# Kernel tuning notes

Measured on AMD Instinct MI355X. Metric: run time of the kernel, lower is better.

The kernel has to match this reference:

```python
import jax, jax.numpy as jnp
import numpy as np

B, S, D = 4, 1568, 1024
H = 16
HD = D // H  # 64


def setup_inputs() -> dict:
    key = jax.random.key(0)
    ks = jax.random.split(key, 9)
    scale = 0.02
    return {
        "hidden_states": jax.random.normal(ks[0], (B, S, D), dtype=jnp.float32),
        "Wq": jax.random.normal(ks[1], (D, D), dtype=jnp.float32) * scale,
        "bq": jnp.zeros((D,), dtype=jnp.float32),
        "Wk": jax.random.normal(ks[2], (D, D), dtype=jnp.float32) * scale,
        "bk": jnp.zeros((D,), dtype=jnp.float32),
        "Wv": jax.random.normal(ks[3], (D, D), dtype=jnp.float32) * scale,
        "bv": jnp.zeros((D,), dtype=jnp.float32),
        "Wp": jax.random.normal(ks[4], (D, D), dtype=jnp.float32) * scale,
        "bp": jnp.zeros((D,), dtype=jnp.float32),
    }


def reference(hidden_states, Wq, bq, Wk, bk, Wv, bv, Wp, bp):
    x = hidden_states  # [B, S, D]
    # Linear projections (torch Linear: x @ W.T + b)
    q = x @ Wq.T + bq
    k = x @ Wk.T + bk
    v = x @ Wv.T + bv
    # split heads: [B, H, S, HD]
    def heads(t):
        return t.reshape(B, S, H, HD).transpose(0, 2, 1, 3)
    q, k, v = heads(q), heads(k), heads(v)
    scale = 1.0 / jnp.sqrt(jnp.asarray(HD, dtype=q.dtype))
    scores = jnp.einsum('bhqd,bhkd->bhqk', q, k) * scale  # [B,H,S,S]
    probs = jax.nn.softmax(scores, axis=-1)
    ctx = jnp.einsum('bhqk,bhkd->bhqd', probs, v)  # [B,H,S,HD]
    ctx = ctx.transpose(0, 2, 1, 3).reshape(B, S, D)
    out = ctx @ Wp.T + bp
    return out
```

## Files before the change

### kernel.cpp

```cpp
#include <hip/hip_runtime.h>
#include <stdint.h>

#define SEQ 1568
#define SEQV 1600
#define DIM 1024
#define NB 4
#define NH 16
#define HD 64

typedef unsigned short u16;
typedef __bf16 bf16x8 __attribute__((ext_vector_type(8)));
typedef __bf16 bf16x4 __attribute__((ext_vector_type(4)));
typedef float f32x4 __attribute__((ext_vector_type(4)));

#define QSCALE 0.18033688011112042f

#define PSTR 72

__device__ __forceinline__ void load_lds16(const u16* g, u16* s) {
  __builtin_amdgcn_global_load_lds((__attribute__((address_space(1))) void*)g,
                                   (__attribute__((address_space(3))) void*)s,
                                   16, 0, 0);
}

#define WAIT_VM(N) asm volatile("s_waitcnt vmcnt(" #N ")" ::: "memory")
#define LGKM0()    asm volatile("s_waitcnt lgkmcnt(0)" ::: "memory")
#define BAR()      do { __builtin_amdgcn_s_barrier(); \
                        __builtin_amdgcn_sched_barrier(0); } while (0)

__global__ __launch_bounds__(256) void cvt_all(
    const float* __restrict__ x,  const float* __restrict__ wq,
    const float* __restrict__ wk, const float* __restrict__ wv,
    const float* __restrict__ wp,
    u16* __restrict__ xb, u16* __restrict__ wqb, u16* __restrict__ wkb,
    u16* __restrict__ wvb, u16* __restrict__ wpb) {
  int i = blockIdx.x * 256 + threadIdx.x;
  const float* src; u16* dst; int off;
  if (i < 1605632)      { src = x;  dst = xb;  off = i; }
  else if (i < 1867776) { src = wq; dst = wqb; off = i - 1605632; }
  else if (i < 2129920) { src = wk; dst = wkb; off = i - 1867776; }
  else if (i < 2392064) { src = wv; dst = wvb; off = i - 2129920; }
  else                  { src = wp; dst = wpb; off = i - 2392064; }
  float4 v = ((const float4*)src)[off];
  union { unsigned long long u; __bf16 h[4]; } o;
  o.h[0] = (__bf16)v.x; o.h[1] = (__bf16)v.y;
  o.h[2] = (__bf16)v.z; o.h[3] = (__bf16)v.w;
  ((unsigned long long*)dst)[off] = o.u;
}

__global__ __launch_bounds__(256) void gemm_qkv(
    const u16* __restrict__ xb,
    const u16* __restrict__ wq, const u16* __restrict__ wk, const u16* __restrict__ wv,
    const float* __restrict__ bq, const float* __restrict__ bk, const float* __restrict__ bv,
    u16* __restrict__ qo, u16* __restrict__ ko, u16* __restrict__ vto) {
  const int bid = blockIdx.x + (blockIdx.y << 3) + blockIdx.z * 416;
  const int logical = (bid & 7) * 156 + (bid >> 3);
  const int byz = logical >> 3;
  const int by  = byz % 52;
  const int z   = byz / 52;
  const int bi  = by / 13;
  const int st  = by % 13;
  const int bn  = (logical & 7) * 128;

  const u16* W = (z == 0) ? wq : (z == 1) ? wk : wv;
  const float* bias = (z == 0) ? bq : (z == 1) ? bk : bv;

  __shared__ __align__(16) u16 sA[3][128 * 32];
  __shared__ __align__(16) u16 sB[3][128 * 32];

  const int tid = threadIdx.x;
  const int wave = tid >> 6;
  const int lane = tid & 63;
  const int l15 = lane & 15;
  const int quad = lane >> 4;
  const int wm = (wave >> 1) * 64;
  const int wn = (wave & 1) * 64;

  const int sr  = lane >> 2;
  const int scs = (((lane & 3) ^ ((lane >> 3) & 3)) << 3);
  const int r0 = wave * 32;

  int ra1 = st * 128 + r0 + sr;       if (ra1 >= SEQ) ra1 = SEQ - 1;
  int ra2 = st * 128 + r0 + 16 + sr;  if (ra2 >= SEQ) ra2 = SEQ - 1;
  const u16* gA1 = xb + (size_t)(bi * SEQ + ra1) * DIM + scs;
  const u16* gA2 = xb + (size_t)(bi * SEQ + ra2) * DIM + scs;
  const u16* gB1 = W + (size_t)(bn + r0 + sr) * DIM + scs;
  const u16* gB2 = gB1 + 16 * DIM;

  f32x4 acc[4][4] = {};
  const int rsw = (l15 >> 1) & 3;

  auto stage = [&](int kk, u16* sAc, u16* sBc) {
    load_lds16(gA1 + kk, sAc + r0 * 32);
    load_lds16(gA2 + kk, sAc + (r0 + 16) * 32);
    load_lds16(gB1 + kk, sBc + r0 * 32);
    load_lds16(gB2 + kk, sBc + (r0 + 16) * 32);
  };

  auto mstep = [&](const u16* sAc, const u16* sBc) {
    bf16x8 a[4], b[4];
#pragma unroll
    for (int mt = 0; mt < 4; mt++)
      a[mt] = *(const bf16x8*)&sAc[(wm + mt * 16 + l15) * 32 + ((quad ^ rsw) << 3)];
#pragma unroll
    for (int nt = 0; nt < 4; nt++)
      b[nt] = *(const bf16x8*)&sBc[(wn + nt * 16 + l15) * 32 + ((quad ^ rsw) << 3)];
#pragma unroll
    for (int mt = 0; mt < 4; mt++)
#pragma unroll
      for (int nt = 0; nt < 4; nt++)
        acc[mt][nt] = __builtin_amdgcn_mfma_f32_16x16x32_bf16(a[mt], b[nt], acc[mt][nt], 0, 0, 0);
  };

  stage(0,  &sA[0][0], &sB[0][0]);
  stage(32, &sA[1][0], &sB[1][0]);
  stage(64, &sA[2][0], &sB[2][0]);

#pragma unroll 1
  for (int t = 0; t < 30; t += 3) {
    WAIT_VM(8); BAR();
    mstep(&sA[0][0], &sB[0][0]);
    LGKM0(); BAR();
    stage((t + 3) * 32, &sA[0][0], &sB[0][0]);

    WAIT_VM(8); BAR();
    mstep(&sA[1][0], &sB[1][0]);
    LGKM0(); BAR();
    stage((t + 4) * 32, &sA[1][0], &sB[1][0]);

    WAIT_VM(8); BAR();
    mstep(&sA[2][0], &sB[2][0]);
    LGKM0(); BAR();
    if (t + 5 < 32) stage((t + 5) * 32, &sA[2][0], &sB[2][0]);
  }
  WAIT_VM(4); BAR();
  mstep(&sA[0][0], &sB[0][0]);
  WAIT_VM(0); BAR();
  mstep(&sA[1][0], &sB[1][0]);

#pragma unroll
  for (int nt = 0; nt < 4; nt++) {
    const int n = bn + wn + nt * 16 + l15;
    const float bia = bias[n];
    const int h = n >> 6, d = n & 63;
#pragma unroll
    for (int mt = 0; mt < 4; mt++) {
      const int sbase = st * 128 + wm + mt * 16 + quad * 4;
#pragma unroll
      for (int r = 0; r < 4; r++) {
        const int s = sbase + r;
        if (s < SEQ) {
          float val = acc[mt][nt][r] + bia;
          if (z == 0) val *= QSCALE;
          const __bf16 o = (__bf16)val;
          if (z == 0)
            *(__bf16*)&qo[(((size_t)(bi * NH + h)) * SEQ + s) * HD + d] = o;
          else if (z == 1)
            *(__bf16*)&ko[(((size_t)(bi * NH + h)) * SEQ + s) * HD + d] = o;
          else
            *(__bf16*)&vto[(((size_t)(bi * NH + h)) * HD + d) * SEQV + s] = o;
        }
      }
    }
  }
}

__global__ __launch_bounds__(256, 3) void attn(
    const u16* __restrict__ q, const u16* __restrict__ k,
    const u16* __restrict__ vt, u16* __restrict__ ctx) {
  const int bid = blockIdx.x;
  const int logical = (bid & 7) * 104 + (bid >> 3);
  const int bh = logical / 13;
  const int qt = logical % 13;
  const int tid = threadIdx.x;
  const int wave = tid >> 6, lane = tid & 63, l15 = lane & 15, quad = lane >> 4;

  __shared__ __align__(16) u16 sK[2][64 * 64];
  __shared__ __align__(16) u16 sV[2][64 * 64];
  __shared__ __align__(16) u16 sP[4][32 * PSTR];

  const u16* qh = q + (size_t)bh * (SEQ * HD);
  const u16* kh = k + (size_t)bh * (SEQ * HD);
  const u16* vh = vt + (size_t)bh * (HD * SEQV);

  bf16x8 aq[2][2];
#pragma unroll
  for (int mt = 0; mt < 2; mt++) {
    int qrow = qt * 128 + wave * 32 + mt * 16 + l15;
    int qr = qrow < SEQ ? qrow : SEQ - 1;
    aq[mt][0] = *(const bf16x8*)&qh[(size_t)qr * HD + quad * 8];
    aq[mt][1] = *(const bf16x8*)&qh[(size_t)qr * HD + 32 + quad * 8];
  }

  f32x4 o[2][4] = {};
  float lsum[2] = {0.0f, 0.0f};

  const int jrow = lane >> 3;
  const int cg = (lane & 7) ^ jrow;
  u16* sPw = sP[wave];
  const int j7 = l15 & 7;
  const int d7 = l15 & 7;

  auto stageKV = [&](int t, int b) {
    const int j0 = t * 64;
    int kr1 = j0 + wave * 16 + jrow;      if (kr1 >= SEQ) kr1 = SEQ - 1;
    int kr2 = j0 + wave * 16 + 8 + jrow;  if (kr2 >= SEQ) kr2 = SEQ - 1;
    load_lds16(&kh[(size_t)kr1 * HD + cg * 8], &sK[b][(wave * 16) * 64]);
    load_lds16(&kh[(size_t)kr2 * HD + cg * 8], &sK[b][(wave * 16 + 8) * 64]);
    load_lds16(&vh[(size_t)(wave * 16 + jrow) * SEQV + j0 + cg * 8], &sV[b][(wave * 16) * 64]);
    load_lds16(&vh[(size_t)(wave * 16 + 8 + jrow) * SEQV + j0 + cg * 8], &sV[b][(wave * 16 + 8) * 64]);
  };

  auto compute_full = [&](int b) {
    const u16* sKc = sK[b];
    const u16* sVc = sV[b];
#pragma unroll
    for (int mt = 0; mt < 2; mt++) {
      f32x4 s[4];
#pragma unroll
      for (int jt = 0; jt < 4; jt++) {
        const int j = jt * 16 + l15;
        bf16x8 b0 = *(const bf16x8*)&sKc[j * 64 + ((quad ^ j7) * 8)];
        bf16x8 b1 = *(const bf16x8*)&sKc[j * 64 + (((4 + quad) ^ j7) * 8)];
        f32x4 acc = {};
        acc = __builtin_amdgcn_mfma_f32_16x16x32_bf16(b0, aq[mt][0], acc, 0, 0, 0);
        acc = __builtin_amdgcn_mfma_f32_16x16x32_bf16(b1, aq[mt][1], acc, 0, 0, 0);
        s[jt] = acc;
      }
#pragma unroll
      for (int jt = 0; jt < 4; jt++) {
        bf16x4 pk;
#pragma unroll
        for (int r = 0; r < 4; r++) {
          float p = __builtin_exp2f(s[jt][r]);
          lsum[mt] += p;
          pk[r] = (__bf16)p;
        }
        *(bf16x4*)&sPw[(mt * 16 + l15) * PSTR + jt * 16 + quad * 4] = pk;
      }
    }

    LGKM0();

#pragma unroll
    for (int kc = 0; kc < 2; kc++) {
      bf16x8 ap0 = *(const bf16x8*)&sPw[l15 * PSTR + kc * 32 + quad * 8];
      bf16x8 ap1 = *(const bf16x8*)&sPw[(16 + l15) * PSTR + kc * 32 + quad * 8];
#pragma unroll
      for (int dt = 0; dt < 4; dt++) {
        bf16x8 bv = *(const bf16x8*)&sVc[(dt * 16 + l15) * 64 + (((kc * 4 + quad) ^ d7) * 8)];
        o[0][dt] = __builtin_amdgcn_mfma_f32_16x16x32_bf16(ap0, bv, o[0][dt], 0, 0, 0);
        o[1][dt] = __builtin_amdgcn_mfma_f32_16x16x32_bf16(ap1, bv, o[1][dt], 0, 0, 0);
      }
    }
  };

  auto compute_tail = [&](int b) {
    const u16* sKc = sK[b];
    const u16* sVc = sV[b];
#pragma unroll
    for (int mt = 0; mt < 2; mt++) {
      f32x4 s[2];
#pragma unroll
      for (int jt = 0; jt < 2; jt++) {
        const int j = jt * 16 + l15;
        bf16x8 b0 = *(const bf16x8*)&sKc[j * 64 + ((quad ^ j7) * 8)];
        bf16x8 b1 = *(const bf16x8*)&sKc[j * 64 + (((4 + quad) ^ j7) * 8)];
        f32x4 acc = {};
        acc = __builtin_amdgcn_mfma_f32_16x16x32_bf16(b0, aq[mt][0], acc, 0, 0, 0);
        acc = __builtin_amdgcn_mfma_f32_16x16x32_bf16(b1, aq[mt][1], acc, 0, 0, 0);
        s[jt] = acc;
      }
#pragma unroll
      for (int jt = 0; jt < 2; jt++) {
        bf16x4 pk;
#pragma unroll
        for (int r = 0; r < 4; r++) {
          float p = __builtin_exp2f(s[jt][r]);
          lsum[mt] += p;
          pk[r] = (__bf16)p;
        }
        *(bf16x4*)&sPw[(mt * 16 + l15) * PSTR + jt * 16 + quad * 4] = pk;
      }
    }

    LGKM0();

    {
      bf16x8 ap0 = *(const bf16x8*)&sPw[l15 * PSTR + quad * 8];
      bf16x8 ap1 = *(const bf16x8*)&sPw[(16 + l15) * PSTR + quad * 8];
#pragma unroll
      for (int dt = 0; dt < 4; dt++) {
        bf16x8 bv = *(const bf16x8*)&sVc[(dt * 16 + l15) * 64 + ((quad ^ d7) * 8)];
        o[0][dt] = __builtin_amdgcn_mfma_f32_16x16x32_bf16(ap0, bv, o[0][dt], 0, 0, 0);
        o[1][dt] = __builtin_amdgcn_mfma_f32_16x16x32_bf16(ap1, bv, o[1][dt], 0, 0, 0);
      }
    }
  };

  stageKV(0, 0);
#pragma unroll 1
  for (int t = 0; t < 25; t++) {
    if (t < 24) {
      stageKV(t + 1, (t + 1) & 1);
      WAIT_VM(4);
    } else {
      WAIT_VM(0);
    }
    BAR();
    if (t < 24) compute_full(t & 1);
    else        compute_tail(t & 1);
    BAR();
  }

  const int bi = bh >> 4, h = bh & 15;
  float Lq[2][4];
#pragma unroll
  for (int mt = 0; mt < 2; mt++) {
    float l = lsum[mt];
    l += __shfl_xor(l, 16);
    l += __shfl_xor(l, 32);
#pragma unroll
    for (int r = 0; r < 4; r++)
      Lq[mt][r] = __shfl(l, quad * 4 + r, 16);
  }
#pragma unroll
  for (int mt = 0; mt < 2; mt++) {
#pragma unroll
    for (int r = 0; r < 4; r++) {
      const int srow = qt * 128 + wave * 32 + mt * 16 + quad * 4 + r;
      if (srow < SEQ) {
        const float inv = 1.0f / Lq[mt][r];
#pragma unroll
        for (int dt = 0; dt < 4; dt++)
          *(__bf16*)&ctx[((size_t)(bi * SEQ + srow)) * DIM + h * HD + dt * 16 + l15] =
              (__bf16)(o[mt][dt][r] * inv);
      }
    }
  }
}

__global__ __launch_bounds__(256) void gemm_out(
    const u16* __restrict__ ctx, const u16* __restrict__ wp,
    const float* __restrict__ bp, float* __restrict__ out) {
  const int bid = blockIdx.x;
  const int logical = (bid & 7) * 49 + (bid >> 3);
  const int bm = (logical >> 3) * 128;
  const int bn = (logical & 7) * 128;

  __shared__ __align__(16) u16 sA[3][128 * 32];
  __shared__ __align__(16) u16 sB[3][128 * 32];

  const int tid = threadIdx.x;
  const int wave = tid >> 6;
  const int lane = tid & 63;
  const int l15 = lane & 15;
  const int quad = lane >> 4;
  const int wm = (wave >> 1) * 64;
  const int wn = (wave & 1) * 64;
  const int sr  = lane >> 2;
  const int scs = (((lane & 3) ^ ((lane >> 3) & 3)) << 3);
  const int r0 = wave * 32;

  const u16* gA1 = ctx + (size_t)(bm + r0 + sr) * DIM + scs;
  const u16* gA2 = gA1 + 16 * DIM;
  const u16* gB1 = wp + (size_t)(bn + r0 + sr) * DIM + scs;
  const u16* gB2 = gB1 + 16 * DIM;

  f32x4 acc[4][4] = {};
  const int rsw = (l15 >> 1) & 3;

  auto stage = [&](int kk, u16* sAc, u16* sBc) {
    load_lds16(gA1 + kk, sAc + r0 * 32);
    load_lds16(gA2 + kk, sAc + (r0 + 16) * 32);
    load_lds16(gB1 + kk, sBc + r0 * 32);
    load_lds16(gB2 + kk, sBc + (r0 + 16) * 32);
  };

  auto mstep = [&](const u16* sAc, const u16* sBc) {
    bf16x8 a[4], b[4];
#pragma unroll
    for (int mt = 0; mt < 4; mt++)
      a[mt] = *(const bf16x8*)&sAc[(wm + mt * 16 + l15) * 32 + ((quad ^ rsw) << 3)];
#pragma unroll
    for (int nt = 0; nt < 4; nt++)
      b[nt] = *(const bf16x8*)&sBc[(wn + nt * 16 + l15) * 32 + ((quad ^ rsw) << 3)];
#pragma unroll
    for (int mt = 0; mt < 4; mt++)
#pragma unroll
      for (int nt = 0; nt < 4; nt++)
        acc[mt][nt] = __builtin_amdgcn_mfma_f32_16x16x32_bf16(a[mt], b[nt], acc[mt][nt], 0, 0, 0);
  };

  stage(0,  &sA[0][0], &sB[0][0]);
  stage(32, &sA[1][0], &sB[1][0]);
  stage(64, &sA[2][0], &sB[2][0]);

#pragma unroll 1
  for (int t = 0; t < 30; t += 3) {
    WAIT_VM(8); BAR();
    mstep(&sA[0][0], &sB[0][0]);
    LGKM0(); BAR();
    stage((t + 3) * 32, &sA[0][0], &sB[0][0]);

    WAIT_VM(8); BAR();
    mstep(&sA[1][0], &sB[1][0]);
    LGKM0(); BAR();
    stage((t + 4) * 32, &sA[1][0], &sB[1][0]);

    WAIT_VM(8); BAR();
    mstep(&sA[2][0], &sB[2][0]);
    LGKM0(); BAR();
    if (t + 5 < 32) stage((t + 5) * 32, &sA[2][0], &sB[2][0]);
  }
  WAIT_VM(4); BAR();
  mstep(&sA[0][0], &sB[0][0]);
  WAIT_VM(0); BAR();
  mstep(&sA[1][0], &sB[1][0]);

#pragma unroll
  for (int nt = 0; nt < 4; nt++) {
    const int n = bn + wn + nt * 16 + l15;
    const float bia = bp[n];
#pragma unroll
    for (int mt = 0; mt < 4; mt++) {
      const int mbase = bm + wm + mt * 16 + quad * 4;
#pragma unroll
      for (int r = 0; r < 4; r++)
        out[(size_t)(mbase + r) * DIM + n] = acc[mt][nt][r] + bia;
    }
  }
}

extern "C" void kernel_launch(void* const* d_in, const int* in_sizes, int n_in,
                              void* d_out, int out_size, void* d_ws, size_t ws_size,
                              hipStream_t stream) {
  const float* x  = (const float*)d_in[0];
  const float* Wq = (const float*)d_in[1];
  const float* bq = (const float*)d_in[2];
  const float* Wk = (const float*)d_in[3];
  const float* bk = (const float*)d_in[4];
  const float* Wv = (const float*)d_in[5];
  const float* bv = (const float*)d_in[6];
  const float* Wp = (const float*)d_in[7];
  const float* bp = (const float*)d_in[8];
  float* out = (float*)d_out;

  char* ws = (char*)d_ws;
  u16* xb   = (u16*)(ws + 0);
  u16* wqb  = (u16*)(ws + 12845056);
  u16* wkb  = (u16*)(ws + 14942208);
  u16* wvb  = (u16*)(ws + 17039360);
  u16* wpb  = (u16*)(ws + 19136512);
  u16* qb   = (u16*)(ws + 21233664);
  u16* kb   = (u16*)(ws + 34078720);
  u16* vtb  = (u16*)(ws + 46923776);
  u16* ctxb = (u16*)(ws + 60030976);

  cvt_all<<<10368, 256, 0, stream>>>(x, Wq, Wk, Wv, Wp, xb, wqb, wkb, wvb, wpb);
  gemm_qkv<<<dim3(8, 52, 3), 256, 0, stream>>>(xb, wqb, wkb, wvb, bq, bk, bv, qb, kb, vtb);
  attn<<<832, 256, 0, stream>>>(qb, kb, vtb, ctxb);
  gemm_out<<<392, 256, 0, stream>>>(ctxb, wpb, bp, out);
}
```

Before: 293.8 us.

## Flatten QKV GEMM rows across batch; single-buffer attention KV with higher occupancy

The QKV projection now tiles over the flattened B*S rows (6272 = 49*128), which removes padded partial tiles per batch and drops the row clamping and bounds checks. Each output row is mapped back to (batch, seq) for the head-split stores. Attention drops double-buffered K/V LDS staging for a single buffer with plain syncthreads, raises launch bounds to 4 blocks per CU, and adds s_setprio around the MFMA sections. The aim is less padding waste and more occupancy to hide latency, at the cost of losing explicit load/compute overlap inside each block.

```diff
diff --git a/kernel.cpp b/kernel.cpp
--- a/kernel.cpp
+++ b/kernel.cpp
@@ -53,14 +53,12 @@
     const u16* __restrict__ wq, const u16* __restrict__ wk, const u16* __restrict__ wv,
     const float* __restrict__ bq, const float* __restrict__ bk, const float* __restrict__ bv,
     u16* __restrict__ qo, u16* __restrict__ ko, u16* __restrict__ vto) {
-  const int bid = blockIdx.x + (blockIdx.y << 3) + blockIdx.z * 416;
-  const int logical = (bid & 7) * 156 + (bid >> 3);
-  const int byz = logical >> 3;
-  const int by  = byz % 52;
-  const int z   = byz / 52;
-  const int bi  = by / 13;
-  const int st  = by % 13;
-  const int bn  = (logical & 7) * 128;
+  const int bid = blockIdx.x;
+  const int logical = (bid & 7) * 147 + (bid >> 3);
+  const int z   = logical / 392;
+  const int rem = logical % 392;
+  const int bm  = (rem >> 3) * 128;
+  const int bn  = (rem & 7) * 128;
 
   const u16* W = (z == 0) ? wq : (z == 1) ? wk : wv;
   const float* bias = (z == 0) ? bq : (z == 1) ? bk : bv;
@@ -80,10 +78,8 @@
   const int scs = (((lane & 3) ^ ((lane >> 3) & 3)) << 3);
   const int r0 = wave * 32;
 
-  int ra1 = st * 128 + r0 + sr;       if (ra1 >= SEQ) ra1 = SEQ - 1;
-  int ra2 = st * 128 + r0 + 16 + sr;  if (ra2 >= SEQ) ra2 = SEQ - 1;
-  const u16* gA1 = xb + (size_t)(bi * SEQ + ra1) * DIM + scs;
-  const u16* gA2 = xb + (size_t)(bi * SEQ + ra2) * DIM + scs;
+  const u16* gA1 = xb + (size_t)(bm + r0 + sr) * DIM + scs;
+  const u16* gA2 = gA1 + 16 * DIM;
   const u16* gB1 = W + (size_t)(bn + r0 + sr) * DIM + scs;
   const u16* gB2 = gB1 + 16 * DIM;
 
@@ -145,27 +141,27 @@
     const int h = n >> 6, d = n & 63;
 #pragma unroll
     for (int mt = 0; mt < 4; mt++) {
-      const int sbase = st * 128 + wm + mt * 16 + quad * 4;
+      const int rbase = bm + wm + mt * 16 + quad * 4;
 #pragma unroll
       for (int r = 0; r < 4; r++) {
-        const int s = sbase + r;
-        if (s < SEQ) {
-          float val = acc[mt][nt][r] + bia;
-          if (z == 0) val *= QSCALE;
-          const __bf16 o = (__bf16)val;
-          if (z == 0)
-            *(__bf16*)&qo[(((size_t)(bi * NH + h)) * SEQ + s) * HD + d] = o;
-          else if (z == 1)
-            *(__bf16*)&ko[(((size_t)(bi * NH + h)) * SEQ + s) * HD + d] = o;
-          else
-            *(__bf16*)&vto[(((size_t)(bi * NH + h)) * HD + d) * SEQV + s] = o;
-        }
-      }
-    }
-  }
-}
-
-__global__ __launch_bounds__(256, 3) void attn(
+        const int row = rbase + r;
+        const int bi = row / SEQ;
+        const int s  = row - bi * SEQ;
+        float val = acc[mt][nt][r] + bia;
+        if (z == 0) val *= QSCALE;
+        const __bf16 o = (__bf16)val;
+        if (z == 0)
+          *(__bf16*)&qo[(((size_t)(bi * NH + h)) * SEQ + s) * HD + d] = o;
+        else if (z == 1)
+          *(__bf16*)&ko[(((size_t)(bi * NH + h)) * SEQ + s) * HD + d] = o;
+        else
+          *(__bf16*)&vto[(((size_t)(bi * NH + h)) * HD + d) * SEQV + s] = o;
+      }
+    }
+  }
+}
+
+__global__ __launch_bounds__(256, 4) void attn(
     const u16* __restrict__ q, const u16* __restrict__ k,
     const u16* __restrict__ vt, u16* __restrict__ ctx) {
   const int bid = blockIdx.x;
@@ -175,8 +171,8 @@
   const int tid = threadIdx.x;
   const int wave = tid >> 6, lane = tid & 63, l15 = lane & 15, quad = lane >> 4;
 
-  __shared__ __align__(16) u16 sK[2][64 * 64];
-  __shared__ __align__(16) u16 sV[2][64 * 64];
+  __shared__ __align__(16) u16 sK[64 * 64];
+  __shared__ __align__(16) u16 sV[64 * 64];
   __shared__ __align__(16) u16 sP[4][32 * PSTR];
 
   const u16* qh = q + (size_t)bh * (SEQ * HD);
@@ -199,34 +195,30 @@
   const int cg = (lane & 7) ^ jrow;
   u16* sPw = sP[wave];
   const int j7 = l15 & 7;
-  const int d7 = l15 & 7;
-
-  auto stageKV = [&](int t, int b) {
-    const int j0 = t * 64;
-    int kr1 = j0 + wave * 16 + jrow;      if (kr1 >= SEQ) kr1 = SEQ - 1;
-    int kr2 = j0 + wave * 16 + 8 + jrow;  if (kr2 >= SEQ) kr2 = SEQ - 1;
-    load_lds16(&kh[(size_t)kr1 * HD + cg * 8], &sK[b][(wave * 16) * 64]);
-    load_lds16(&kh[(size_t)kr2 * HD + cg * 8], &sK[b][(wave * 16 + 8) * 64]);
-    load_lds16(&vh[(size_t)(wave * 16 + jrow) * SEQV + j0 + cg * 8], &sV[b][(wave * 16) * 64]);
-    load_lds16(&vh[(size_t)(wave * 16 + 8 + jrow) * SEQV + j0 + cg * 8], &sV[b][(wave * 16 + 8) * 64]);
-  };
-
-  auto compute_full = [&](int b) {
-    const u16* sKc = sK[b];
-    const u16* sVc = sV[b];
+
+  for (int j0 = 0; j0 < 1536; j0 += 64) {
+    __syncthreads();
+    load_lds16(&kh[(size_t)(j0 + wave * 16 + jrow) * HD + cg * 8], &sK[(wave * 16) * 64]);
+    load_lds16(&kh[(size_t)(j0 + wave * 16 + 8 + jrow) * HD + cg * 8], &sK[(wave * 16 + 8) * 64]);
+    load_lds16(&vh[(size_t)(wave * 16 + jrow) * SEQV + j0 + cg * 8], &sV[(wave * 16) * 64]);
+    load_lds16(&vh[(size_t)(wave * 16 + 8 + jrow) * SEQV + j0 + cg * 8], &sV[(wave * 16 + 8) * 64]);
+    __syncthreads();
+
 #pragma unroll
     for (int mt = 0; mt < 2; mt++) {
       f32x4 s[4];
+      __builtin_amdgcn_s_setprio(1);
 #pragma unroll
       for (int jt = 0; jt < 4; jt++) {
         const int j = jt * 16 + l15;
-        bf16x8 b0 = *(const bf16x8*)&sKc[j * 64 + ((quad ^ j7) * 8)];
-        bf16x8 b1 = *(const bf16x8*)&sKc[j * 64 + (((4 + quad) ^ j7) * 8)];
+        bf16x8 b0 = *(const bf16x8*)&sK[j * 64 + ((quad ^ j7) * 8)];
+        bf16x8 b1 = *(const bf16x8*)&sK[j * 64 + (((4 + quad) ^ j7) * 8)];
         f32x4 acc = {};
         acc = __builtin_amdgcn_mfma_f32_16x16x32_bf16(b0, aq[mt][0], acc, 0, 0, 0);
         acc = __builtin_amdgcn_mfma_f32_16x16x32_bf16(b1, aq[mt][1], acc, 0, 0, 0);
         s[jt] = acc;
       }
+      __builtin_amdgcn_s_setprio(0);
 #pragma unroll
       for (int jt = 0; jt < 4; jt++) {
         bf16x4 pk;
@@ -242,30 +234,41 @@
 
     LGKM0();
 
+    __builtin_amdgcn_s_setprio(1);
 #pragma unroll
     for (int kc = 0; kc < 2; kc++) {
       bf16x8 ap0 = *(const bf16x8*)&sPw[l15 * PSTR + kc * 32 + quad * 8];
       bf16x8 ap1 = *(const bf16x8*)&sPw[(16 + l15) * PSTR + kc * 32 + quad * 8];
 #pragma unroll
       for (int dt = 0; dt < 4; dt++) {
-        bf16x8 bv = *(const bf16x8*)&sVc[(dt * 16 + l15) * 64 + (((kc * 4 + quad) ^ d7) * 8)];
+        const int d7 = l15 & 7;
+        bf16x8 bv = *(const bf16x8*)&sV[(dt * 16 + l15) * 64 + (((kc * 4 + quad) ^ d7) * 8)];
         o[0][dt] = __builtin_amdgcn_mfma_f32_16x16x32_bf16(ap0, bv, o[0][dt], 0, 0, 0);
         o[1][dt] = __builtin_amdgcn_mfma_f32_16x16x32_bf16(ap1, bv, o[1][dt], 0, 0, 0);
       }
     }
-  };
-
-  auto compute_tail = [&](int b) {
-    const u16* sKc = sK[b];
-    const u16* sVc = sV[b];
+    __builtin_amdgcn_s_setprio(0);
+  }
+
+  {
+    const int j0 = 1536;
+    __syncthreads();
+    if (wave < 2) {
+      load_lds16(&kh[(size_t)(j0 + wave * 16 + jrow) * HD + cg * 8], &sK[(wave * 16) * 64]);
+      load_lds16(&kh[(size_t)(j0 + wave * 16 + 8 + jrow) * HD + cg * 8], &sK[(wave * 16 + 8) * 64]);
+    }
+    load_lds16(&vh[(size_t)(wave * 16 + jrow) * SEQV + j0 + cg * 8], &sV[(wave * 16) * 64]);
+    load_lds16(&vh[(size_t)(wave * 16 + 8 + jrow) * SEQV + j0 + cg * 8], &sV[(wave * 16 + 8) * 64]);
+    __syncthreads();
+
 #pragma unroll
     for (int mt = 0; mt < 2; mt++) {
       f32x4 s[2];
 #pragma unroll
       for (int jt = 0; jt < 2; jt++) {
         const int j = jt * 16 + l15;
-        bf16x8 b0 = *(const bf16x8*)&sKc[j * 64 + ((quad ^ j7) * 8)];
-        bf16x8 b1 = *(const bf16x8*)&sKc[j * 64 + (((4 + quad) ^ j7) * 8)];
+        bf16x8 b0 = *(const bf16x8*)&sK[j * 64 + ((quad ^ j7) * 8)];
+        bf16x8 b1 = *(const bf16x8*)&sK[j * 64 + (((4 + quad) ^ j7) * 8)];
         f32x4 acc = {};
         acc = __builtin_amdgcn_mfma_f32_16x16x32_bf16(b0, aq[mt][0], acc, 0, 0, 0);
         acc = __builtin_amdgcn_mfma_f32_16x16x32_bf16(b1, aq[mt][1], acc, 0, 0, 0);
@@ -291,26 +294,12 @@
       bf16x8 ap1 = *(const bf16x8*)&sPw[(16 + l15) * PSTR + quad * 8];
 #pragma unroll
       for (int dt = 0; dt < 4; dt++) {
-        bf16x8 bv = *(const bf16x8*)&sVc[(dt * 16 + l15) * 64 + ((quad ^ d7) * 8)];
+        const int d7 = l15 & 7;
+        bf16x8 bv = *(const bf16x8*)&sV[(dt * 16 + l15) * 64 + ((quad ^ d7) * 8)];
         o[0][dt] = __builtin_amdgcn_mfma_f32_16x16x32_bf16(ap0, bv, o[0][dt], 0, 0, 0);
         o[1][dt] = __builtin_amdgcn_mfma_f32_16x16x32_bf16(ap1, bv, o[1][dt], 0, 0, 0);
       }
     }
-  };
-
-  stageKV(0, 0);
-#pragma unroll 1
-  for (int t = 0; t < 25; t++) {
-    if (t < 24) {
-      stageKV(t + 1, (t + 1) & 1);
-      WAIT_VM(4);
-    } else {
-      WAIT_VM(0);
-    }
-    BAR();
-    if (t < 24) compute_full(t & 1);
-    else        compute_tail(t & 1);
-    BAR();
   }
 
   const int bi = bh >> 4, h = bh & 15;
@@ -458,7 +447,7 @@
   u16* ctxb = (u16*)(ws + 60030976);
 
   cvt_all<<<10368, 256, 0, stream>>>(x, Wq, Wk, Wv, Wp, xb, wqb, wkb, wvb, wpb);
-  gemm_qkv<<<dim3(8, 52, 3), 256, 0, stream>>>(xb, wqb, wkb, wvb, bq, bk, bv, qb, kb, vtb);
+  gemm_qkv<<<1176, 256, 0, stream>>>(xb, wqb, wkb, wvb, bq, bk, bv, qb, kb, vtb);
   attn<<<832, 256, 0, stream>>>(qb, kb, vtb, ctxb);
   gemm_out<<<392, 256, 0, stream>>>(ctxb, wpb, bp, out);
 }
```

New measurement: 292.9 us. Within noise of the previous version (-0.3%).
